# Kernel optimization log

Measured on AMD Instinct MI355X. Metric: run time of the kernel, lower is better.

## Reference

```python
import jax, jax.numpy as jnp
import numpy as np
from jax import lax

# IVF+PQ search (FAISS IVF1024,PQ8x8 with nprobe=32, by_residual=False variant):
# 1) coarse quantizer: L2 distance of each query to nlist centroids, keep top nprobe lists
# 2) ADC: per-query LUT of squared distances between query subvectors and PQ codebooks,
#    database distance = sum over subquantizers of LUT gathered at the stored codes
# 3) mask database vectors whose IVF list was not probed, return indices of top_k smallest

NPROBE = 32  # top_n_centroids
BIG = jnp.float32(1e30)


def setup_inputs() -> dict:
    key = jax.random.key(0)
    ks = jax.random.split(key, 5)
    Q, D = 256, 128
    M, K = 8, 256          # pq_subvecs, 2**pq_nbits
    dsub = D // M          # 16
    nlist = 1024
    N = 250_000            # database size
    queries = jax.random.normal(ks[0], (Q, D), dtype=jnp.float32)
    centroids = jax.random.normal(ks[1], (nlist, D), dtype=jnp.float32)
    codebooks = jax.random.normal(ks[2], (M, K, dsub), dtype=jnp.float32)
    db_codes = jax.random.randint(ks[3], (N, M), 0, K, dtype=jnp.int32)
    db_list = jax.random.randint(ks[4], (N,), 0, nlist, dtype=jnp.int32)
    return {"queries": queries, "centroids": centroids, "codebooks": codebooks,
            "db_codes": db_codes, "db_list": db_list, "top_k": 100}


def _masked_adc_distances(queries, centroids, codebooks, db_codes, db_list):
    Q, D = queries.shape
    nlist = centroids.shape[0]
    M, K, dsub = codebooks.shape
    # ---- coarse quantizer: ||q - c||^2 over [Q, nlist] ----
    coarse = (jnp.sum(queries * queries, -1, keepdims=True)
              + jnp.sum(centroids * centroids, -1)[None, :]
              - 2.0 * queries @ centroids.T)
    _, probed = lax.top_k(-coarse, NPROBE)                      # [Q, NPROBE] list ids
    probe_mask = jnp.zeros((Q, nlist), dtype=bool).at[
        jnp.arange(Q)[:, None], probed].set(True)               # [Q, nlist]
    allowed = probe_mask[:, db_list]                            # [Q, N]
    # ---- PQ ADC lookup table: ||q_sub - codeword||^2, [Q, M, K] ----
    qs = queries.reshape(Q, M, dsub)
    lut = (jnp.sum(qs * qs, -1)[:, :, None]
           + jnp.sum(codebooks * codebooks, -1)[None, :, :]
           - 2.0 * jnp.einsum('qmd,mkd->qmk', qs, codebooks))   # [Q, M, K]
    # ---- accumulate gathered LUT entries over subquantizers ----
    dist = lut[:, 0, db_codes[:, 0]]                            # [Q, N]
    for m in range(1, M):
        dist = dist + lut[:, m, db_codes[:, m]]
    return jnp.where(allowed, dist, BIG)


def reference(queries, centroids, codebooks, db_codes, db_list, top_k):
    dist = _masked_adc_distances(queries, centroids, codebooks, db_codes, db_list)
    _, indices = lax.top_k(-dist, top_k)                        # smallest distances
    return indices
```

## Files before the change

### kernel.cpp

```cpp
#include <hip/hip_runtime.h>

#define DDIM 128
#define MSUB 8
#define KCODE 256
#define DSUB 16
#define NLIST 1024
#define NPROBE 32
#define TOPK 100
#define HBINS 4096
#define COLL_CAP 2048
#define RCAP 12
#define SCHUNK 4096


__device__ __forceinline__ float xla_sumsq128(const float* x) {
  float s[16];
  #pragma unroll
  for (int j = 0; j < 16; ++j) {
    float p0 = __fmul_rn(x[j],       x[j]);
    float p1 = __fmul_rn(x[j + 16],  x[j + 16]);
    float p2 = __fmul_rn(x[j + 32],  x[j + 32]);
    float p3 = __fmul_rn(x[j + 48],  x[j + 48]);
    float p4 = __fmul_rn(x[j + 64],  x[j + 64]);
    float p5 = __fmul_rn(x[j + 80],  x[j + 80]);
    float p6 = __fmul_rn(x[j + 96],  x[j + 96]);
    float p7 = __fmul_rn(x[j + 112], x[j + 112]);
    float r0 = __fadd_rn(p0, p4);
    float r1 = __fadd_rn(p1, p5);
    float r2 = __fadd_rn(p2, p6);
    float r3 = __fadd_rn(p3, p7);
    s[j] = __fadd_rn(__fadd_rn(r0, r1), __fadd_rn(r2, r3));
  }
  float a[8], b[4], c[2];
  #pragma unroll
  for (int j = 0; j < 8; ++j) a[j] = __fadd_rn(s[j], s[j + 8]);
  #pragma unroll
  for (int j = 0; j < 4; ++j) b[j] = __fadd_rn(a[j], a[j + 4]);
  #pragma unroll
  for (int j = 0; j < 2; ++j) c[j] = __fadd_rn(b[j], b[j + 2]);
  return __fadd_rn(c[0], c[1]);
}

__device__ __forceinline__ float xla_sumsq128_g(const float* __restrict__ cr) {
  float r0[16], r1[16], t01[16];
  #pragma unroll
  for (int j = 0; j < 16; ++j)
    r0[j] = __fadd_rn(__fmul_rn(cr[j], cr[j]), __fmul_rn(cr[j + 64], cr[j + 64]));
  #pragma unroll
  for (int j = 0; j < 16; ++j)
    r1[j] = __fadd_rn(__fmul_rn(cr[j + 16], cr[j + 16]), __fmul_rn(cr[j + 80], cr[j + 80]));
  #pragma unroll
  for (int j = 0; j < 16; ++j) t01[j] = __fadd_rn(r0[j], r1[j]);
  #pragma unroll
  for (int j = 0; j < 16; ++j)
    r0[j] = __fadd_rn(__fmul_rn(cr[j + 32], cr[j + 32]), __fmul_rn(cr[j + 96], cr[j + 96]));
  #pragma unroll
  for (int j = 0; j < 16; ++j)
    r1[j] = __fadd_rn(__fmul_rn(cr[j + 48], cr[j + 48]), __fmul_rn(cr[j + 112], cr[j + 112]));
  float s[16];
  #pragma unroll
  for (int j = 0; j < 16; ++j) s[j] = __fadd_rn(t01[j], __fadd_rn(r0[j], r1[j]));
  float a[8], b[4], c[2];
  #pragma unroll
  for (int j = 0; j < 8; ++j) a[j] = __fadd_rn(s[j], s[j + 8]);
  #pragma unroll
  for (int j = 0; j < 4; ++j) b[j] = __fadd_rn(a[j], a[j + 4]);
  #pragma unroll
  for (int j = 0; j < 2; ++j) c[j] = __fadd_rn(b[j], b[j + 2]);
  return __fadd_rn(c[0], c[1]);
}

__device__ __forceinline__ float xla_sumsq16(const float* x) {
  float p[16];
  #pragma unroll
  for (int j = 0; j < 16; ++j) p[j] = __fmul_rn(x[j], x[j]);
  float s8[8], s4[4], s2[2];
  #pragma unroll
  for (int j = 0; j < 8; ++j) s8[j] = __fadd_rn(p[j], p[j + 8]);
  #pragma unroll
  for (int j = 0; j < 4; ++j) s4[j] = __fadd_rn(s8[j], s8[j + 4]);
  #pragma unroll
  for (int j = 0; j < 2; ++j) s2[j] = __fadd_rn(s4[j], s4[j + 2]);
  return __fadd_rn(s2[0], s2[1]);
}

__device__ __forceinline__ float chain_dot16(const float* a, const float* b) {
  float dot = 0.f;
  #pragma unroll
  for (int d = 0; d < DSUB; ++d) dot = __fmaf_rn(a[d], b[d], dot);
  return dot;
}

__device__ __forceinline__ float adc_dist(const float* lut, unsigned long long code) {
  float d = lut[(unsigned)(code & 255ULL)];
  d = __fadd_rn(d, lut[256  + (unsigned)((code >> 8)  & 255ULL)]);
  d = __fadd_rn(d, lut[512  + (unsigned)((code >> 16) & 255ULL)]);
  d = __fadd_rn(d, lut[768  + (unsigned)((code >> 24) & 255ULL)]);
  d = __fadd_rn(d, lut[1024 + (unsigned)((code >> 32) & 255ULL)]);
  d = __fadd_rn(d, lut[1280 + (unsigned)((code >> 40) & 255ULL)]);
  d = __fadd_rn(d, lut[1536 + (unsigned)((code >> 48) & 255ULL)]);
  d = __fadd_rn(d, lut[1792 + (unsigned)((code >> 56) & 255ULL)]);
  return d;
}

__device__ __forceinline__ unsigned block_scan_incl(unsigned v, volatile unsigned* wsum,
                                                    int t, int nwaves) {
  int lane = t & 63, wid = t >> 6;
  #pragma unroll
  for (int off = 1; off < 64; off <<= 1) {
    unsigned u = __shfl_up(v, off, 64);
    if (lane >= off) v += u;
  }
  if (lane == 63) wsum[wid] = v;
  __syncthreads();
  if (wid == 0 && lane < nwaves) {
    unsigned wv = wsum[lane];
    #pragma unroll
    for (int off = 1; off < 16; off <<= 1) {
      unsigned u = __shfl_up(wv, off, 64);
      if (lane >= off) wv += u;
    }
    wsum[lane] = wv;
  }
  __syncthreads();
  return v + (wid > 0 ? wsum[wid - 1] : 0u);
}

__global__ __launch_bounds__(256) void k_coarse_lut(const float* __restrict__ queries,
                                                    const float* __restrict__ centroids,
                                                    const float* __restrict__ codebooks,
                                                    const int* __restrict__ db_list, int N,
                                                    float* __restrict__ lut_g,
                                                    int* __restrict__ probed,
                                                    unsigned* __restrict__ counts) {
  const int qi = blockIdx.x;
  const int t = threadIdx.x;
  __shared__ float qs[DDIM];
  __shared__ unsigned hist[HBINS];
  __shared__ unsigned long long coll[512];
  __shared__ unsigned wsum[4];
  __shared__ unsigned scnt;
  __shared__ int sT32;
  if (t < DDIM) qs[t] = queries[qi * DDIM + t];
  for (int i = t; i < HBINS; i += 256) hist[i] = 0;
  if (t == 0) { scnt = 0; sT32 = HBINS - 1; }
  __syncthreads();

  for (int j = 0; j < MSUB; ++j) {
    int idx = j * KCODE + t;
    const float* cb = codebooks + (size_t)idx * DSUB;
    const float* qsub = qs + j * DSUB;
    float cbv[DSUB], qv[DSUB];
    #pragma unroll
    for (int d = 0; d < DSUB; ++d) { cbv[d] = cb[d]; qv[d] = qsub[d]; }
    const float qq16 = xla_sumsq16(qv);
    const float cc16 = xla_sumsq16(cbv);
    const float dot16 = chain_dot16(qv, cbv);
    lut_g[(size_t)qi * (MSUB * KCODE) + idx] =
        __fsub_rn(__fadd_rn(qq16, cc16), __fmul_rn(2.0f, dot16));
  }

  const float qq = xla_sumsq128(qs);
  unsigned long long keys[4];
  #pragma unroll
  for (int w = 0; w < 4; ++w) {
    int c = t + 256 * w;
    const float* cr = centroids + (size_t)c * DDIM;
    const float cc = xla_sumsq128_g(cr);
    float dot = 0.f;
    #pragma unroll
    for (int d = 0; d < DDIM; ++d) dot = __fmaf_rn(qs[d], cr[d], dot);
    float dist = __fsub_rn(__fadd_rn(qq, cc), __fmul_rn(2.0f, dot));
    unsigned bits = __float_as_uint(dist);
    keys[w] = ((unsigned long long)bits << 32) | (unsigned)c;
    atomicAdd(&hist[bits >> 19], 1u);
  }
  __syncthreads();

  unsigned mysum = 0;
  #pragma unroll
  for (int i = 0; i < 16; ++i) mysum += hist[t * 16 + i];
  unsigned incl = block_scan_incl(mysum, wsum, t, 4);
  unsigned excl = incl - mysum;
  if (excl < NPROBE && NPROBE <= incl) {
    unsigned c2 = excl;
    for (int i = 0; i < 16; ++i) {
      unsigned h = hist[t * 16 + i];
      if (c2 + h >= NPROBE) { sT32 = t * 16 + i; break; }
      c2 += h;
    }
  }
  __syncthreads();
  const int T32 = sT32;
  #pragma unroll
  for (int w = 0; w < 4; ++w) {
    if ((int)(keys[w] >> 51) <= T32) {
      unsigned p = atomicAdd(&scnt, 1u);
      if (p < 512) coll[p] = keys[w];
    }
  }
  __syncthreads();
  unsigned cnt = scnt; if (cnt > 512) cnt = 512;
  for (unsigned i = t; i < cnt; i += 256) {
    unsigned long long key = coll[i];
    unsigned r = 0;
    for (unsigned j = 0; j < cnt; ++j) r += (coll[j] < key) ? 1u : 0u;
    if (r < NPROBE) probed[qi * NPROBE + r] = (int)(key & 0xffffffffULL);
  }
  __syncthreads();

  for (int i = t; i < NLIST; i += 256) hist[i] = 0;
  __syncthreads();
  for (int n = qi * 256 + t; n < N; n += 256 * 256)
    atomicAdd(&hist[db_list[n]], 1u);
  __syncthreads();
  for (int i = t; i < NLIST; i += 256)
    if (hist[i]) atomicAdd(&counts[i], hist[i]);
}

__global__ __launch_bounds__(1024) void k_scan(const unsigned* __restrict__ counts,
                                               unsigned* __restrict__ bstart) {
  __shared__ unsigned s[NLIST];
  const int t = threadIdx.x;
  unsigned mine = counts[t];
  s[t] = mine;
  __syncthreads();
  for (int off = 1; off < NLIST; off <<= 1) {
    unsigned v = (t >= off) ? s[t - off] : 0u;
    __syncthreads();
    s[t] += v;
    __syncthreads();
  }
  bstart[t + 1] = s[t];
  if (t == 0) bstart[0] = 0;
}

__global__ __launch_bounds__(256) void k_scatter(const int* __restrict__ db_list,
                                                 const int* __restrict__ db_codes, int N,
                                                 const unsigned* __restrict__ bstart,
                                                 unsigned* __restrict__ cursor,
                                                 int4* __restrict__ pack) {
  __shared__ unsigned lhist[NLIST], lbase[NLIST];
  const int t = threadIdx.x;
  const int base = blockIdx.x * SCHUNK;
  for (int i = t; i < NLIST; i += 256) lhist[i] = 0;
  __syncthreads();
  #pragma unroll
  for (int k = 0; k < SCHUNK / 256; ++k) {
    int n = base + k * 256 + t;
    if (n < N) atomicAdd(&lhist[db_list[n]], 1u);
  }
  __syncthreads();
  for (int i = t; i < NLIST; i += 256) {
    unsigned cnt = lhist[i];
    if (cnt) lbase[i] = bstart[i] + atomicAdd(&cursor[i], cnt);
    lhist[i] = 0;
  }
  __syncthreads();
  #pragma unroll
  for (int k = 0; k < SCHUNK / 256; ++k) {
    int n = base + k * 256 + t;
    if (n < N) {
      int l = db_list[n];
      unsigned pos = lbase[l] + atomicAdd(&lhist[l], 1u);
      const int4* cp = (const int4*)(db_codes + (size_t)n * MSUB);
      int4 c0 = cp[0], c1 = cp[1];
      unsigned lo = (unsigned)(c0.x & 255) | ((unsigned)(c0.y & 255) << 8) |
                    ((unsigned)(c0.z & 255) << 16) | ((unsigned)(c0.w & 255) << 24);
      unsigned hi = (unsigned)(c1.x & 255) | ((unsigned)(c1.y & 255) << 8) |
                    ((unsigned)(c1.z & 255) << 16) | ((unsigned)(c1.w & 255) << 24);
      pack[pos] = make_int4((int)lo, (int)hi, n, 0);
    }
  }
}

__global__ __launch_bounds__(1024, 1) void k_search(const float* __restrict__ lut_g,
                                                    const int* __restrict__ probed,
                                                    const unsigned* __restrict__ bstart,
                                                    const int4* __restrict__ pack,
                                                    int* __restrict__ out) {
  const int qi = blockIdx.x;
  const int t = threadIdx.x;
  __shared__ float lut_s[MSUB * KCODE];
  __shared__ unsigned hist[HBINS];
  __shared__ unsigned long long coll[COLL_CAP];
  __shared__ unsigned pstart[NPROBE], pcum[NPROBE + 1];
  __shared__ unsigned wsum[16];
  __shared__ unsigned scnt;
  __shared__ int sT, sCb, sT2;

  for (int i = t; i < MSUB * KCODE; i += 1024) lut_s[i] = lut_g[(size_t)qi * (MSUB * KCODE) + i];
  if (t < NPROBE) {
    int l = probed[qi * NPROBE + t];
    unsigned s0 = bstart[l];
    pstart[t] = s0;
    pcum[t + 1] = bstart[l + 1] - s0;
  }
  for (int i = t; i < HBINS; i += 1024) hist[i] = 0;
  if (t == 0) { scnt = 0; sT = HBINS - 1; sCb = 0; sT2 = HBINS - 1; }
  __syncthreads();
  if (t == 0) {
    unsigned acc = 0;
    pcum[0] = 0;
    for (int j = 1; j <= NPROBE; ++j) { acc += pcum[j]; pcum[j] = acc; }
  }
  __syncthreads();
  const unsigned total = pcum[NPROBE];

  unsigned regbits[RCAP];
  {
    int s = 0;
    for (unsigned g = t; g < total; g += 1024, ++s) {
      int lo = 0, hi = NPROBE;
      while (hi - lo > 1) { int mid = (lo + hi) >> 1; if (pcum[mid] <= g) lo = mid; else hi = mid; }
      unsigned addr = pstart[lo] + (g - pcum[lo]);
      int4 w = pack[addr];
      unsigned long long code = (unsigned)w.x | ((unsigned long long)(unsigned)w.y << 32);
      unsigned bits = __float_as_uint(adc_dist(lut_s, code));
      if (s < RCAP) regbits[s] = bits;
      atomicAdd(&hist[bits >> 19], 1u);
    }
  }
  __syncthreads();

  {
    unsigned mysum = 0;
    #pragma unroll
    for (int i = 0; i < 4; ++i) mysum += hist[t * 4 + i];
    unsigned incl = block_scan_incl(mysum, wsum, t, 16);
    unsigned excl = incl - mysum;
    if (excl < TOPK && TOPK <= incl) {
      unsigned c = excl;
      #pragma unroll
      for (int i = 0; i < 4; ++i) {
        unsigned h = hist[t * 4 + i];
        if (c + h >= TOPK) { sT = t * 4 + i; sCb = (int)c; break; }
        c += h;
      }
    }
  }
  __syncthreads();
  const int T = sT;
  const unsigned cbelow = (unsigned)sCb;
  for (int i = t; i < HBINS; i += 1024) hist[i] = 0;
  __syncthreads();

  {
    int s = 0;
    for (unsigned g = t; g < total; g += 1024, ++s) {
      unsigned bits;
      if (s < RCAP) bits = regbits[s];
      else {
        int lo = 0, hi = NPROBE;
        while (hi - lo > 1) { int mid = (lo + hi) >> 1; if (pcum[mid] <= g) lo = mid; else hi = mid; }
        int4 w = pack[pstart[lo] + (g - pcum[lo])];
        unsigned long long code = (unsigned)w.x | ((unsigned long long)(unsigned)w.y << 32);
        bits = __float_as_uint(adc_dist(lut_s, code));
      }
      if ((int)(bits >> 19) == T) atomicAdd(&hist[(bits >> 7) & 0xFFFu], 1u);
    }
  }
  __syncthreads();
  {
    const unsigned R2 = TOPK - cbelow;
    unsigned mysum = 0;
    #pragma unroll
    for (int i = 0; i < 4; ++i) mysum += hist[t * 4 + i];
    unsigned incl = block_scan_incl(mysum, wsum, t, 16);
    unsigned excl = incl - mysum;
    if (excl < R2 && R2 <= incl) {
      unsigned c = excl;
      #pragma unroll
      for (int i = 0; i < 4; ++i) {
        unsigned h = hist[t * 4 + i];
        if (c + h >= R2) { sT2 = t * 4 + i; break; }
        c += h;
      }
    }
  }
  __syncthreads();
  const int T2 = sT2;

  {
    int s = 0;
    for (unsigned g = t; g < total; g += 1024, ++s) {
      unsigned bits;
      int lo = -1;
      if (s < RCAP) bits = regbits[s];
      else {
        int l2 = 0, hi = NPROBE;
        while (hi - l2 > 1) { int mid = (l2 + hi) >> 1; if (pcum[mid] <= g) l2 = mid; else hi = mid; }
        lo = l2;
        int4 w = pack[pstart[lo] + (g - pcum[lo])];
        unsigned long long code = (unsigned)w.x | ((unsigned long long)(unsigned)w.y << 32);
        bits = __float_as_uint(adc_dist(lut_s, code));
      }
      int bin = (int)(bits >> 19);
      int sub = (int)((bits >> 7) & 0xFFFu);
      if (bin < T || (bin == T && sub <= T2)) {
        if (lo < 0) {
          int l2 = 0, hi = NPROBE;
          while (hi - l2 > 1) { int mid = (l2 + hi) >> 1; if (pcum[mid] <= g) l2 = mid; else hi = mid; }
          lo = l2;
        }
        unsigned n = (unsigned)pack[pstart[lo] + (g - pcum[lo])].z;
        unsigned p = atomicAdd(&scnt, 1u);
        if (p < COLL_CAP) coll[p] = ((unsigned long long)bits << 32) | n;
      }
    }
  }
  __syncthreads();

  unsigned cnt = scnt;
  if (cnt > COLL_CAP) cnt = COLL_CAP;
  for (unsigned i = t; i < cnt; i += 1024) {
    unsigned long long key = coll[i];
    unsigned r = 0;
    for (unsigned j = 0; j < cnt; ++j) r += (coll[j] < key) ? 1u : 0u;
    if (r < TOPK) out[qi * TOPK + r] = (int)(key & 0xffffffffULL);
  }
}

extern "C" void kernel_launch(void* const* d_in, const int* in_sizes, int n_in,
                              void* d_out, int out_size, void* d_ws, size_t ws_size,
                              hipStream_t stream) {
  const float* queries   = (const float*)d_in[0];
  const float* centroids = (const float*)d_in[1];
  const float* codebooks = (const float*)d_in[2];
  const int*   db_codes  = (const int*)d_in[3];
  const int*   db_list   = (const int*)d_in[4];
  const int N = in_sizes[4];
  const int Q = in_sizes[0] / DDIM;
  int* out = (int*)d_out;

  char* p = (char*)d_ws;
  float* lut_g = (float*)p;        p += (size_t)Q * MSUB * KCODE * 4;
  int* probed_g = (int*)p;         p += (size_t)Q * NPROBE * 4;
  unsigned* counts = (unsigned*)p; p += NLIST * 4;
  unsigned* cursor = (unsigned*)p; p += NLIST * 4;
  unsigned* bstart = (unsigned*)p; p += (NLIST + 4) * 4;
  int4* pack = (int4*)p;           p += (size_t)N * 16;

  hipMemsetAsync(counts, 0, (size_t)NLIST * 4 * 2, stream);

  k_coarse_lut<<<Q, 256, 0, stream>>>(queries, centroids, codebooks, db_list, N,
                                      lut_g, probed_g, counts);
  k_scan<<<1, 1024, 0, stream>>>(counts, bstart);
  k_scatter<<<(N + SCHUNK - 1) / SCHUNK, 256, 0, stream>>>(db_list, db_codes, N,
                                                           bstart, cursor, pack);
  k_search<<<Q, 1024, 0, stream>>>(lut_g, probed_g, bstart, pack, out);
}
```

Measured before the change: 140.3 us.

## Drop second-level histogram refinement and vectorize centroid loads in coarse stage

Removes the second radix-histogram pass over the probed candidates in the search kernel and collects every candidate whose top-bin is at or below the threshold bin directly. This cuts a full extra pass over the probed codes, a block scan and two barriers. In exchange it may collect many more candidates into the capped collection buffer, which can overflow it and makes the final ranking sort larger. The coarse-quantizer stage now loads each centroid with float4 reads into registers and reuses the shared sumsq routine, and SCHUNK is reduced.

```diff
diff --git a/kernel.cpp b/kernel.cpp
--- a/kernel.cpp
+++ b/kernel.cpp
@@ -10,7 +10,7 @@
 #define HBINS 4096
 #define COLL_CAP 2048
 #define RCAP 12
-#define SCHUNK 4096
+#define SCHUNK 1024
 
 
 __device__ __forceinline__ float xla_sumsq128(const float* x) {
@@ -31,35 +31,6 @@
     float r3 = __fadd_rn(p3, p7);
     s[j] = __fadd_rn(__fadd_rn(r0, r1), __fadd_rn(r2, r3));
   }
-  float a[8], b[4], c[2];
-  #pragma unroll
-  for (int j = 0; j < 8; ++j) a[j] = __fadd_rn(s[j], s[j + 8]);
-  #pragma unroll
-  for (int j = 0; j < 4; ++j) b[j] = __fadd_rn(a[j], a[j + 4]);
-  #pragma unroll
-  for (int j = 0; j < 2; ++j) c[j] = __fadd_rn(b[j], b[j + 2]);
-  return __fadd_rn(c[0], c[1]);
-}
-
-__device__ __forceinline__ float xla_sumsq128_g(const float* __restrict__ cr) {
-  float r0[16], r1[16], t01[16];
-  #pragma unroll
-  for (int j = 0; j < 16; ++j)
-    r0[j] = __fadd_rn(__fmul_rn(cr[j], cr[j]), __fmul_rn(cr[j + 64], cr[j + 64]));
-  #pragma unroll
-  for (int j = 0; j < 16; ++j)
-    r1[j] = __fadd_rn(__fmul_rn(cr[j + 16], cr[j + 16]), __fmul_rn(cr[j + 80], cr[j + 80]));
-  #pragma unroll
-  for (int j = 0; j < 16; ++j) t01[j] = __fadd_rn(r0[j], r1[j]);
-  #pragma unroll
-  for (int j = 0; j < 16; ++j)
-    r0[j] = __fadd_rn(__fmul_rn(cr[j + 32], cr[j + 32]), __fmul_rn(cr[j + 96], cr[j + 96]));
-  #pragma unroll
-  for (int j = 0; j < 16; ++j)
-    r1[j] = __fadd_rn(__fmul_rn(cr[j + 48], cr[j + 48]), __fmul_rn(cr[j + 112], cr[j + 112]));
-  float s[16];
-  #pragma unroll
-  for (int j = 0; j < 16; ++j) s[j] = __fadd_rn(t01[j], __fadd_rn(r0[j], r1[j]));
   float a[8], b[4], c[2];
   #pragma unroll
   for (int j = 0; j < 8; ++j) a[j] = __fadd_rn(s[j], s[j + 8]);
@@ -166,10 +137,16 @@
   for (int w = 0; w < 4; ++w) {
     int c = t + 256 * w;
     const float* cr = centroids + (size_t)c * DDIM;
-    const float cc = xla_sumsq128_g(cr);
+    float cbuf[DDIM];
+    #pragma unroll
+    for (int d = 0; d < DDIM; d += 4) {
+      float4 cv = *(const float4*)(cr + d);
+      cbuf[d] = cv.x; cbuf[d + 1] = cv.y; cbuf[d + 2] = cv.z; cbuf[d + 3] = cv.w;
+    }
+    const float cc = xla_sumsq128(cbuf);
     float dot = 0.f;
     #pragma unroll
-    for (int d = 0; d < DDIM; ++d) dot = __fmaf_rn(qs[d], cr[d], dot);
+    for (int d = 0; d < DDIM; ++d) dot = __fmaf_rn(qs[d], cbuf[d], dot);
     float dist = __fsub_rn(__fadd_rn(qq, cc), __fmul_rn(2.0f, dot));
     unsigned bits = __float_as_uint(dist);
     keys[w] = ((unsigned long long)bits << 32) | (unsigned)c;
@@ -287,7 +264,7 @@
   __shared__ unsigned pstart[NPROBE], pcum[NPROBE + 1];
   __shared__ unsigned wsum[16];
   __shared__ unsigned scnt;
-  __shared__ int sT, sCb, sT2;
+  __shared__ int sT;
 
   for (int i = t; i < MSUB * KCODE; i += 1024) lut_s[i] = lut_g[(size_t)qi * (MSUB * KCODE) + i];
   if (t < NPROBE) {
@@ -297,7 +274,7 @@
     pcum[t + 1] = bstart[l + 1] - s0;
   }
   for (int i = t; i < HBINS; i += 1024) hist[i] = 0;
-  if (t == 0) { scnt = 0; sT = HBINS - 1; sCb = 0; sT2 = HBINS - 1; }
+  if (t == 0) { scnt = 0; sT = HBINS - 1; }
   __syncthreads();
   if (t == 0) {
     unsigned acc = 0;
@@ -334,52 +311,13 @@
       #pragma unroll
       for (int i = 0; i < 4; ++i) {
         unsigned h = hist[t * 4 + i];
-        if (c + h >= TOPK) { sT = t * 4 + i; sCb = (int)c; break; }
+        if (c + h >= TOPK) { sT = t * 4 + i; break; }
         c += h;
       }
     }
   }
   __syncthreads();
   const int T = sT;
-  const unsigned cbelow = (unsigned)sCb;
-  for (int i = t; i < HBINS; i += 1024) hist[i] = 0;
-  __syncthreads();
-
-  {
-    int s = 0;
-    for (unsigned g = t; g < total; g += 1024, ++s) {
-      unsigned bits;
-      if (s < RCAP) bits = regbits[s];
-      else {
-        int lo = 0, hi = NPROBE;
-        while (hi - lo > 1) { int mid = (lo + hi) >> 1; if (pcum[mid] <= g) lo = mid; else hi = mid; }
-        int4 w = pack[pstart[lo] + (g - pcum[lo])];
-        unsigned long long code = (unsigned)w.x | ((unsigned long long)(unsigned)w.y << 32);
-        bits = __float_as_uint(adc_dist(lut_s, code));
-      }
-      if ((int)(bits >> 19) == T) atomicAdd(&hist[(bits >> 7) & 0xFFFu], 1u);
-    }
-  }
-  __syncthreads();
-  {
-    const unsigned R2 = TOPK - cbelow;
-    unsigned mysum = 0;
-    #pragma unroll
-    for (int i = 0; i < 4; ++i) mysum += hist[t * 4 + i];
-    unsigned incl = block_scan_incl(mysum, wsum, t, 16);
-    unsigned excl = incl - mysum;
-    if (excl < R2 && R2 <= incl) {
-      unsigned c = excl;
-      #pragma unroll
-      for (int i = 0; i < 4; ++i) {
-        unsigned h = hist[t * 4 + i];
-        if (c + h >= R2) { sT2 = t * 4 + i; break; }
-        c += h;
-      }
-    }
-  }
-  __syncthreads();
-  const int T2 = sT2;
 
   {
     int s = 0;
@@ -395,9 +333,7 @@
         unsigned long long code = (unsigned)w.x | ((unsigned long long)(unsigned)w.y << 32);
         bits = __float_as_uint(adc_dist(lut_s, code));
       }
-      int bin = (int)(bits >> 19);
-      int sub = (int)((bits >> 7) & 0xFFFu);
-      if (bin < T || (bin == T && sub <= T2)) {
+      if ((int)(bits >> 19) <= T) {
         if (lo < 0) {
           int l2 = 0, hi = NPROBE;
           while (hi - l2 > 1) { int mid = (l2 + hi) >> 1; if (pcum[mid] <= g) l2 = mid; else hi = mid; }
```

Result: faster. 135.6 us (-3.4%).
